# Performance work log

Measured on AMD Instinct MI355X. Metric: run time of the kernel, lower is better.

Reference implementation:

```python
import jax, jax.numpy as jnp
import numpy as np

B, CIN, COUT, H, W, K, PAD, STRIDE = 32, 64, 64, 224, 224, 3, 1, 1


def setup_inputs() -> dict:
    key = jax.random.key(0)
    kx, kw, kb = jax.random.split(key, 3)
    x = jax.random.normal(kx, (B, CIN, H, W), dtype=jnp.float32)
    weight = jax.random.normal(kw, (COUT, CIN, K, K), dtype=jnp.float32)
    bias = jax.random.normal(kb, (COUT,), dtype=jnp.float32)
    return {"x": x, "weight": weight, "bias": bias}


def reference(x, weight, bias):
    # Binarize weights with sign (matches torch.sign: sign(0) == 0).
    w_bin = jnp.sign(weight)
    out = jax.lax.conv_general_dilated(
        x, w_bin,
        window_strides=(STRIDE, STRIDE),
        padding=[(PAD, PAD), (PAD, PAD)],
        dimension_numbers=("NCHW", "OIHW", "NCHW"),
    )
    return out + bias[None, :, None, None]
```

## Files before the change

### kernel.cpp

```cpp
#include <hip/hip_runtime.h>

#define BATCH 32
#define CIN_  64
#define COUT_ 64
#define H_    224
#define W_    224
#define HW_   (H_*W_)

#define HT     2
#define WTILE  112
#define XS_P   116
#define NROWS  (HT+2)
#define NG     7

typedef __bf16 bf16x4 __attribute__((ext_vector_type(4)));
typedef __bf16 bf16x8 __attribute__((ext_vector_type(8)));
typedef float  f32x4  __attribute__((ext_vector_type(4)));
typedef float  f32x16 __attribute__((ext_vector_type(16)));

__global__ void bc_prep(const float* __restrict__ w, __bf16* __restrict__ wp) {
    int gid = blockIdx.x * 256 + threadIdx.x;
    if (gid >= COUT_ * CIN_ * 9) return;
    int co  = gid / (CIN_ * 9);
    int rem = gid - co * (CIN_ * 9);
    int ci  = rem / 9;
    int t   = rem - ci * 9;
    float v = w[gid];
    float s = (v > 0.0f) ? 1.0f : ((v < 0.0f) ? -1.0f : 0.0f);
    wp[t * (COUT_ * CIN_) + co * CIN_ + ci] = (__bf16)s;
}

__global__ __launch_bounds__(256, 2)
void bc_main(const float* __restrict__ x, const __bf16* __restrict__ wp,
             const float* __restrict__ bias, float* __restrict__ out) {
    __shared__ __attribute__((aligned(16))) __bf16 xs[NROWS * XS_P * 64];

    const int htile = blockIdx.x;
    const int wt    = blockIdx.y;
    const int bb    = blockIdx.z;
    const int h0 = htile * HT;
    const int w0 = wt * WTILE;

    const int tid  = threadIdx.x;
    const int lane = tid & 63;
    const int wave = tid >> 6;
    const int ct   = wave & 1;
    const int gs   = wave >> 1;
    const int col  = lane & 31;
    const int kh   = lane >> 5;

    bf16x8 afrag[36];
    {
        const int m = ct * 32 + col;
        #pragma unroll
        for (int s = 0; s < 36; ++s) {
            const int tap = s >> 2;
            const int cib = (s & 3) * 16 + kh * 8;
            afrag[s] = *(const bf16x8*)(wp + tap * (COUT_ * CIN_) + m * CIN_ + cib);
        }
    }
    float biasr[16];
    #pragma unroll
    for (int r = 0; r < 16; ++r)
        biasr[r] = bias[ct * 32 + 4 * kh + (r & 3) + 8 * (r >> 2)];

    const int cig   = tid >> 4;
    const int ci0   = cig * 4;
    const int cc    = cig >> 1;
    const int chalf = (cig & 1) * 4;

    #pragma unroll
    for (int r = 0; r < NROWS; ++r) {
        const int hin = h0 - 1 + r;
        const bool rowok = (hin >= 0) && (hin < H_);
        const float* src = x + (size_t)bb * CIN_ * HW_ + (size_t)hin * W_;
        #pragma unroll
        for (int s = 0; s < 2; ++s) {
            const int pxg = (tid & 15) + s * 16;
            const int wbase = w0 - 4 + pxg * 4;
            float vv[4][4];
            #pragma unroll
            for (int j = 0; j < 4; ++j) {
                const float* pr = src + (size_t)(ci0 + j) * HW_ + wbase;
                if (rowok && wbase >= 0 && wbase + 3 < W_) {
                    float4 f = *(const float4*)pr;
                    vv[j][0] = f.x; vv[j][1] = f.y; vv[j][2] = f.z; vv[j][3] = f.w;
                } else {
                    #pragma unroll
                    for (int i = 0; i < 4; ++i) {
                        const int wg = wbase + i;
                        vv[j][i] = (rowok && wg >= 0 && wg < W_) ? pr[i] : 0.0f;
                    }
                }
            }
            #pragma unroll
            for (int i = 0; i < 4; ++i) {
                const int p = pxg * 4 + i - 3;
                if (p >= 0 && p < XS_P) {
                    bf16x4 pk;
                    pk[0] = (__bf16)vv[0][i];
                    pk[1] = (__bf16)vv[1][i];
                    pk[2] = (__bf16)vv[2][i];
                    pk[3] = (__bf16)vv[3][i];
                    const int cp = cc ^ ((p >> 1) & 7);
                    *(bf16x4*)&xs[(r * XS_P + p) * 64 + cp * 8 + chalf] = pk;
                }
            }
        }
    }
    __syncthreads();

    const int hh  = col >> 4;
    const int pxl = col & 15;
    const int swz0 = ((pxl + 0) >> 1) & 7;
    const int swz1 = ((pxl + 1) >> 1) & 7;
    const int swz2 = ((pxl + 2) >> 1) & 7;

    for (int g = gs; g < NG; g += 2) {
        f32x16 acc = {};
        #pragma unroll
        for (int s = 0; s < 36; ++s) {
            const int tap = s >> 2;
            const int dh  = tap / 3;
            const int dw  = tap - dh * 3;
            const int swz = (dw == 0) ? swz0 : ((dw == 1) ? swz1 : swz2);
            const int c   = (s & 3) * 2 + kh;
            const int cp  = c ^ swz;
            const int pin = g * 16 + pxl + dw;
            const bf16x8* bsrc =
                (const bf16x8*)&xs[((hh + dh) * XS_P + pin) * 64 + cp * 8];
            acc = __builtin_amdgcn_mfma_f32_32x32x16_bf16(afrag[s], *bsrc, acc, 0, 0, 0);
        }
        float* op = out + ((size_t)bb * COUT_ + ct * 32 + 4 * kh) * (size_t)HW_
                        + (size_t)(h0 + hh) * W_ + (w0 + g * 16 + pxl);
        #pragma unroll
        for (int r = 0; r < 16; ++r) {
            const int co_r = (r & 3) + 8 * (r >> 2);
            op[(size_t)co_r * HW_] = acc[r] + biasr[r];
        }
    }
}

extern "C" void kernel_launch(void* const* d_in, const int* in_sizes, int n_in,
                              void* d_out, int out_size, void* d_ws, size_t ws_size,
                              hipStream_t stream) {
    const float* x    = (const float*)d_in[0];
    const float* w    = (const float*)d_in[1];
    const float* bias = (const float*)d_in[2];
    float* out = (float*)d_out;
    __bf16* wp = (__bf16*)d_ws;

    bc_prep<<<dim3((COUT_ * CIN_ * 9 + 255) / 256), dim3(256), 0, stream>>>(w, wp);
    bc_main<<<dim3(H_ / HT, W_ / WTILE, BATCH), dim3(256), 0, stream>>>(x, wp, bias, out);
}
```

Before: 932.8 us.

## Make blocks persistent over row strips with a ring-buffered, register-prefetched input pipeline

Each block now handles a strip of 28 row-pairs instead of a single row-pair. Input rows live in a 4-slot circular LDS buffer, and the next two rows are loaded into registers while MFMAs run on the current rows. Blocks grow to 512 threads, and four wave-pairs split the pixel groups. This is meant to remove the 2x halo reload overhead and the per-block A-fragment and bias reloads, and to overlap global loads with compute. In exchange the grid drops to 256 blocks, which risks low occupancy and tail imbalance (7 groups over 4 selectors), and adds two barriers per iteration and more register pressure.

```diff
diff --git a/kernel.cpp b/kernel.cpp
--- a/kernel.cpp
+++ b/kernel.cpp
@@ -10,12 +10,12 @@
 #define HT     2
 #define WTILE  112
 #define XS_P   116
-#define NROWS  (HT+2)
 #define NG     7
+#define HSTRIP 28
+#define ROWSZ  (XS_P*64)
 
 typedef __bf16 bf16x4 __attribute__((ext_vector_type(4)));
 typedef __bf16 bf16x8 __attribute__((ext_vector_type(8)));
-typedef float  f32x4  __attribute__((ext_vector_type(4)));
 typedef float  f32x16 __attribute__((ext_vector_type(16)));
 
 __global__ void bc_prep(const float* __restrict__ w, __bf16* __restrict__ wp) {
@@ -30,22 +30,22 @@
     wp[t * (COUT_ * CIN_) + co * CIN_ + ci] = (__bf16)s;
 }
 
-__global__ __launch_bounds__(256, 2)
+__global__ __launch_bounds__(512, 2)
 void bc_main(const float* __restrict__ x, const __bf16* __restrict__ wp,
              const float* __restrict__ bias, float* __restrict__ out) {
-    __shared__ __attribute__((aligned(16))) __bf16 xs[NROWS * XS_P * 64];
+    __shared__ __attribute__((aligned(16))) __bf16 xs[4 * ROWSZ];
 
-    const int htile = blockIdx.x;
-    const int wt    = blockIdx.y;
-    const int bb    = blockIdx.z;
-    const int h0 = htile * HT;
+    const int hs = blockIdx.x;
+    const int wt = blockIdx.y;
+    const int bb = blockIdx.z;
+    const int h0 = hs * (HSTRIP * HT);
     const int w0 = wt * WTILE;
 
     const int tid  = threadIdx.x;
     const int lane = tid & 63;
     const int wave = tid >> 6;
     const int ct   = wave & 1;
-    const int gs   = wave >> 1;
+    const int gsel = wave >> 1;
     const int col  = lane & 31;
     const int kh   = lane >> 5;
 
@@ -64,80 +64,110 @@
     for (int r = 0; r < 16; ++r)
         biasr[r] = bias[ct * 32 + 4 * kh + (r & 3) + 8 * (r >> 2)];
 
-    const int cig   = tid >> 4;
+    const int rsel  = tid >> 8;
+    const int t8    = tid & 255;
+    const int pxg0  = t8 & 15;
+    const int cig   = t8 >> 4;
     const int ci0   = cig * 4;
     const int cc    = cig >> 1;
     const int chalf = (cig & 1) * 4;
 
-    #pragma unroll
-    for (int r = 0; r < NROWS; ++r) {
-        const int hin = h0 - 1 + r;
+    float pb[2][4][4];
+
+    auto issue2 = [&](int rowbase) {
+        const int hin = rowbase + rsel;
         const bool rowok = (hin >= 0) && (hin < H_);
         const float* src = x + (size_t)bb * CIN_ * HW_ + (size_t)hin * W_;
         #pragma unroll
         for (int s = 0; s < 2; ++s) {
-            const int pxg = (tid & 15) + s * 16;
-            const int wbase = w0 - 4 + pxg * 4;
-            float vv[4][4];
+            const int wbase = w0 - 4 + (pxg0 + s * 16) * 4;
             #pragma unroll
             for (int j = 0; j < 4; ++j) {
                 const float* pr = src + (size_t)(ci0 + j) * HW_ + wbase;
                 if (rowok && wbase >= 0 && wbase + 3 < W_) {
                     float4 f = *(const float4*)pr;
-                    vv[j][0] = f.x; vv[j][1] = f.y; vv[j][2] = f.z; vv[j][3] = f.w;
+                    pb[s][j][0] = f.x; pb[s][j][1] = f.y;
+                    pb[s][j][2] = f.z; pb[s][j][3] = f.w;
                 } else {
                     #pragma unroll
                     for (int i = 0; i < 4; ++i) {
                         const int wg = wbase + i;
-                        vv[j][i] = (rowok && wg >= 0 && wg < W_) ? pr[i] : 0.0f;
+                        pb[s][j][i] = (rowok && wg >= 0 && wg < W_) ? pr[i] : 0.0f;
                     }
                 }
             }
+        }
+    };
+
+    auto commit2 = [&](int rowbase) {
+        const int slot = (rowbase + rsel) & 3;
+        __bf16* dst = xs + slot * ROWSZ;
+        #pragma unroll
+        for (int s = 0; s < 2; ++s) {
+            const int pxg = pxg0 + s * 16;
             #pragma unroll
             for (int i = 0; i < 4; ++i) {
                 const int p = pxg * 4 + i - 3;
                 if (p >= 0 && p < XS_P) {
                     bf16x4 pk;
-                    pk[0] = (__bf16)vv[0][i];
-                    pk[1] = (__bf16)vv[1][i];
-                    pk[2] = (__bf16)vv[2][i];
-                    pk[3] = (__bf16)vv[3][i];
+                    pk[0] = (__bf16)pb[s][0][i];
+                    pk[1] = (__bf16)pb[s][1][i];
+                    pk[2] = (__bf16)pb[s][2][i];
+                    pk[3] = (__bf16)pb[s][3][i];
                     const int cp = cc ^ ((p >> 1) & 7);
-                    *(bf16x4*)&xs[(r * XS_P + p) * 64 + cp * 8 + chalf] = pk;
+                    *(bf16x4*)&dst[p * 64 + cp * 8 + chalf] = pk;
                 }
             }
         }
-    }
+    };
+
+    issue2(h0 - 1); commit2(h0 - 1);
+    issue2(h0 + 1); commit2(h0 + 1);
+    issue2(h0 + 3);
     __syncthreads();
 
     const int hh  = col >> 4;
     const int pxl = col & 15;
-    const int swz0 = ((pxl + 0) >> 1) & 7;
-    const int swz1 = ((pxl + 1) >> 1) & 7;
-    const int swz2 = ((pxl + 2) >> 1) & 7;
+    int swz[3];
+    #pragma unroll
+    for (int dw = 0; dw < 3; ++dw) swz[dw] = ((pxl + dw) >> 1) & 7;
 
-    for (int g = gs; g < NG; g += 2) {
-        f32x16 acc = {};
+    #pragma unroll 1
+    for (int t = 0; t < HSTRIP; ++t) {
+        const int h0t = h0 + 2 * t;
+        int rbase[3];
         #pragma unroll
-        for (int s = 0; s < 36; ++s) {
-            const int tap = s >> 2;
-            const int dh  = tap / 3;
-            const int dw  = tap - dh * 3;
-            const int swz = (dw == 0) ? swz0 : ((dw == 1) ? swz1 : swz2);
-            const int c   = (s & 3) * 2 + kh;
-            const int cp  = c ^ swz;
-            const int pin = g * 16 + pxl + dw;
-            const bf16x8* bsrc =
-                (const bf16x8*)&xs[((hh + dh) * XS_P + pin) * 64 + cp * 8];
-            acc = __builtin_amdgcn_mfma_f32_32x32x16_bf16(afrag[s], *bsrc, acc, 0, 0, 0);
+        for (int dh = 0; dh < 3; ++dh)
+            rbase[dh] = ((h0t - 1 + hh + dh) & 3) * ROWSZ;
+
+        for (int g = gsel; g < NG; g += 4) {
+            f32x16 acc = {};
+            #pragma unroll
+            for (int s = 0; s < 36; ++s) {
+                const int tap = s >> 2;
+                const int dh  = tap / 3;
+                const int dw  = tap - dh * 3;
+                const int c   = (s & 3) * 2 + kh;
+                const int cp  = c ^ swz[dw];
+                const int pin = g * 16 + pxl + dw;
+                const bf16x8* bsrc =
+                    (const bf16x8*)&xs[rbase[dh] + pin * 64 + cp * 8];
+                acc = __builtin_amdgcn_mfma_f32_32x32x16_bf16(afrag[s], *bsrc, acc, 0, 0, 0);
+            }
+            float* op = out + ((size_t)bb * COUT_ + ct * 32 + 4 * kh) * (size_t)HW_
+                            + (size_t)(h0t + hh) * W_ + (w0 + g * 16 + pxl);
+            #pragma unroll
+            for (int r = 0; r < 16; ++r) {
+                const int co_r = (r & 3) + 8 * (r >> 2);
+                op[(size_t)co_r * HW_] = acc[r] + biasr[r];
+            }
         }
-        float* op = out + ((size_t)bb * COUT_ + ct * 32 + 4 * kh) * (size_t)HW_
-                        + (size_t)(h0 + hh) * W_ + (w0 + g * 16 + pxl);
-        #pragma unroll
-        for (int r = 0; r < 16; ++r) {
-            const int co_r = (r & 3) + 8 * (r >> 2);
-            op[(size_t)co_r * HW_] = acc[r] + biasr[r];
-        }
+
+        if (t == HSTRIP - 1) break;
+        __syncthreads();
+        commit2(h0t + 3);
+        if (t < HSTRIP - 2) issue2(h0t + 5);
+        __syncthreads();
     }
 }
 
@@ -151,5 +181,5 @@
     __bf16* wp = (__bf16*)d_ws;
 
     bc_prep<<<dim3((COUT_ * CIN_ * 9 + 255) / 256), dim3(256), 0, stream>>>(w, wp);
-    bc_main<<<dim3(H_ / HT, W_ / WTILE, BATCH), dim3(256), 0, stream>>>(x, wp, bias, out);
+    bc_main<<<dim3(224 / (HSTRIP * HT), W_ / WTILE, BATCH), dim3(512), 0, stream>>>(x, wp, bias, out);
 }
```

New measurement: 1.038 ms. +11.3%, slower.
